# Optimization experiments

Hardware: AMD Instinct MI355X
Metric: run time of the kernel (lower is better)

The kernel has to match this reference:

```python
import jax, jax.numpy as jnp
import numpy as np

N = 12288
IN_DIM = 256
OUT_DIM = 128
NEG_SLOPE = 0.01  # torch nn.LeakyReLU default


def setup_inputs() -> dict:
    key = jax.random.key(0)
    k1, k2, k3, k4, k5 = jax.random.split(key, 5)
    adj_mx = jax.random.randint(k1, (N, N), 0, 2, dtype=jnp.int32)
    input_features = jax.random.normal(k2, (N, IN_DIM), dtype=jnp.float32)
    # Linear(in_dim, out_dim): weight [out, in], bias [out]
    W = jax.random.normal(k3, (OUT_DIM, IN_DIM), dtype=jnp.float32) / np.sqrt(IN_DIM)
    b = jax.random.normal(k4, (OUT_DIM,), dtype=jnp.float32) * 0.01
    phi = jax.random.normal(k5, (2 * OUT_DIM, 1), dtype=jnp.float32)
    return {"adj_mx": adj_mx, "input_features": input_features, "W": W, "b": b, "phi": phi}


def reference(adj_mx, input_features, W, b, phi):
    # projection (dropout is identity in eval): [N, out]
    new_features = input_features @ W.T + b
    # additive attention halves: (N,1) + (1,N) -> [N,N]
    first_half = new_features @ phi[:OUT_DIM]          # [N,1]
    second_half = (new_features @ phi[OUT_DIM:]).T     # [1,N]
    similarity = jax.nn.leaky_relu(first_half + second_half, NEG_SLOPE)
    # adjacency with self-loops; mask non-edges to -1e20
    adj_hat = adj_mx.astype(jnp.float32) + jnp.eye(adj_mx.shape[0], dtype=jnp.float32)
    masked = jnp.where(adj_hat > 0, similarity, jnp.float32(-1e20))
    att = jax.nn.softmax(masked, axis=1)               # row-wise softmax [N,N]
    out = att @ new_features                           # [N, out]
    return jax.nn.leaky_relu(out, NEG_SLOPE)
```

## Files before the change

### kernel.cpp

```cpp
#include <hip/hip_runtime.h>
#include <hip/hip_bf16.h>

#define N_NODES 12288
#define IN_DIM 256
#define OUT_DIM 128
#define NEG 0.01f
#define LOG2E 1.44269504088896340736f
#define NSPLIT 4
#define JSPAN (N_NODES / NSPLIT)
#define ROWS_PER_BLK 64
#define TILE_J 32
#define NTILES (JSPAN / TILE_J)

typedef __attribute__((ext_vector_type(8))) short short8;
typedef __attribute__((ext_vector_type(4))) float f32x4;

__device__ __forceinline__ float fast_exp2(float x) {
#if __has_builtin(__builtin_amdgcn_exp2f)
  return __builtin_amdgcn_exp2f(x);
#else
  return exp2f(x);
#endif
}

__device__ __forceinline__ unsigned short f2bf(float x) {
  unsigned u = __float_as_uint(x);
  unsigned r = (u + 0x7FFFu + ((u >> 16) & 1u)) >> 16;
  return (unsigned short)r;
}

__global__ __launch_bounds__(256) void k1_proj(
    const float* __restrict__ X, const float* __restrict__ W,
    const float* __restrict__ bias, float* __restrict__ nf,
    unsigned short* __restrict__ Vt) {
  __shared__ float Xs[32][40];
  __shared__ float Ws[32][136];
  const int t = threadIdx.x;
  const int i0 = blockIdx.x * 32;
  const int tx = t & 31, ty = t >> 5;
  float acc[4][4] = {};
  for (int k0 = 0; k0 < IN_DIM; k0 += 32) {
    __syncthreads();
    {
      int r = t >> 3, kq = (t & 7) * 4;
      float4 xv = *(const float4*)&X[(size_t)(i0 + r) * IN_DIM + k0 + kq];
      Xs[kq + 0][r] = xv.x; Xs[kq + 1][r] = xv.y;
      Xs[kq + 2][r] = xv.z; Xs[kq + 3][r] = xv.w;
    }
#pragma unroll
    for (int q = 0; q < 4; ++q) {
      int idx = t + q * 256;
      int c = idx >> 3, kq = (idx & 7) * 4;
      float4 wv = *(const float4*)&W[(size_t)c * IN_DIM + k0 + kq];
      Ws[kq + 0][c] = wv.x; Ws[kq + 1][c] = wv.y;
      Ws[kq + 2][c] = wv.z; Ws[kq + 3][c] = wv.w;
    }
    __syncthreads();
#pragma unroll
    for (int kk = 0; kk < 32; ++kk) {
      float4 a = *(const float4*)&Xs[kk][ty * 4];
      float4 bv = *(const float4*)&Ws[kk][tx * 4];
      float av[4] = {a.x, a.y, a.z, a.w};
      float bw[4] = {bv.x, bv.y, bv.z, bv.w};
#pragma unroll
      for (int r = 0; r < 4; ++r)
#pragma unroll
        for (int c = 0; c < 4; ++c) acc[r][c] += av[r] * bw[c];
    }
  }
  float4 bv = *(const float4*)&bias[tx * 4];
  float bb[4] = {bv.x, bv.y, bv.z, bv.w};
#pragma unroll
  for (int r = 0; r < 4; ++r) {
    int i = i0 + ty * 4 + r;
    float o[4];
#pragma unroll
    for (int c = 0; c < 4; ++c) {
      o[c] = acc[r][c] + bb[c];
      Vt[(size_t)(tx * 4 + c) * N_NODES + i] = f2bf(o[c]);
    }
    *(float4*)&nf[(size_t)i * OUT_DIM + tx * 4] = *(float4*)o;
  }
}

__global__ __launch_bounds__(64) void k2_fs(
    const float* __restrict__ nf, const float* __restrict__ phi,
    float* __restrict__ f, float* __restrict__ s, unsigned* __restrict__ smax) {
  const int i = blockIdx.x, l = threadIdx.x;
  float2 v = *(const float2*)&nf[(size_t)i * OUT_DIM + 2 * l];
  float2 p1 = *(const float2*)&phi[2 * l];
  float2 p2 = *(const float2*)&phi[OUT_DIM + 2 * l];
  float fp = v.x * p1.x + v.y * p1.y;
  float sp = v.x * p2.x + v.y * p2.y;
#pragma unroll
  for (int o = 32; o; o >>= 1) {
    fp += __shfl_xor(fp, o);
    sp += __shfl_xor(sp, o);
  }
  if (l == 0) {
    f[i] = fp; s[i] = sp;
    unsigned u = __float_as_uint(sp);
    unsigned key = (u & 0x80000000u) ? ~u : (u | 0x80000000u);
    atomicMax(smax, key);
  }
}

__global__ __launch_bounds__(256) void k3_attn(
    const int* __restrict__ adj, const unsigned short* __restrict__ Vt,
    const float* __restrict__ f, const float* __restrict__ s,
    const unsigned* __restrict__ smaxk,
    float* __restrict__ pacc, float* __restrict__ pden) {
  __shared__ float s_lds[JSPAN];
  __shared__ __align__(16) unsigned short Vt_lds[128 * 40];
  __shared__ __align__(16) unsigned short P_lds[64 * 40];
  __shared__ float den_lds[64][4];
  const int t = threadIdx.x;
  const int sp = blockIdx.x & (NSPLIT - 1);
  const int rb = blockIdx.x >> 2;
  const int j0g = sp * JSPAN;
  const int i_loc = t >> 2, jg = t & 3;
  const int i = rb * ROWS_PER_BLK + i_loc;
#pragma unroll
  for (int q = 0; q < 3; ++q) {
    int idx = (t + q * 256) * 4;
    *(float4*)&s_lds[idx] = *(const float4*)&s[j0g + idx];
  }
  unsigned key = *smaxk;
  unsigned u = (key & 0x80000000u) ? (key ^ 0x80000000u) : ~key;
  const float smaxv = __uint_as_float(u);
  const float fi = f[i];
  const float xm = fi + smaxv;
  const float m = fmaxf(xm, NEG * xm);
  const float em = m * LOG2E;
  const int diag_loc = i - j0g;
  float dsum = 0.f;
  f32x4 acc[4][2] = {};
  const int w = t >> 6, l = t & 63;
  const int slot = 8 * (l >> 4);
  const int sd = t >> 1, sh = (t & 1) * 16;
  const unsigned short* vsrc_base = Vt + (size_t)sd * N_NODES + j0g + sh;
  unsigned short* vdst = &Vt_lds[sd * 40 + sh];
  const int* adj_base = adj + (size_t)i * N_NODES + j0g + jg * 8;
  __syncthreads();
  for (int tile = 0; tile < NTILES; ++tile) {
    const int jl0 = tile * TILE_J;
    int4 v0 = *(const int4*)(vsrc_base + jl0);
    int4 v1 = *(const int4*)(vsrc_base + jl0 + 8);
    *(int4*)vdst = v0;
    *(int4*)(vdst + 8) = v1;
    const int jl = jl0 + jg * 8;
    int4 a0 = *(const int4*)(adj_base + jl0);
    int4 a1 = *(const int4*)(adj_base + jl0 + 4);
    float4 sA = *(const float4*)&s_lds[jl];
    float4 sB = *(const float4*)&s_lds[jl + 4];
    const int adjv[8] = {a0.x, a0.y, a0.z, a0.w, a1.x, a1.y, a1.z, a1.w};
    const float sv[8] = {sA.x, sA.y, sA.z, sA.w, sB.x, sB.y, sB.z, sB.w};
    short8 pv;
#pragma unroll
    for (int q = 0; q < 8; ++q) {
      float x = fi + sv[q];
      float xl = fmaxf(x, NEG * x);
      float e = fast_exp2(__builtin_fmaf(xl, LOG2E, -em));
      bool edge = (adjv[q] > 0) || ((jl + q) == diag_loc);
      float p = edge ? e : 0.f;
      dsum += p;
      pv[q] = (short)f2bf(p);
    }
    *(short8*)&P_lds[i_loc * 40 + 8 * jg] = pv;
    __syncthreads();
    short8 af[4];
#pragma unroll
    for (int mt = 0; mt < 4; ++mt)
      af[mt] = *(const short8*)&P_lds[(16 * mt + (l & 15)) * 40 + slot];
#pragma unroll
    for (int nt = 0; nt < 2; ++nt) {
      short8 bfr = *(const short8*)&Vt_lds[(32 * w + 16 * nt + (l & 15)) * 40 + slot];
#pragma unroll
      for (int mt = 0; mt < 4; ++mt)
        acc[mt][nt] = __builtin_amdgcn_mfma_f32_16x16x32_bf16(af[mt], bfr, acc[mt][nt], 0, 0, 0);
    }
    __syncthreads();
  }
  den_lds[i_loc][jg] = dsum;
  __syncthreads();
  if (t < 64) {
    pden[sp * N_NODES + rb * ROWS_PER_BLK + t] =
        den_lds[t][0] + den_lds[t][1] + den_lds[t][2] + den_lds[t][3];
  }
  float* pa = pacc + (size_t)sp * N_NODES * OUT_DIM;
#pragma unroll
  for (int mt = 0; mt < 4; ++mt)
#pragma unroll
    for (int nt = 0; nt < 2; ++nt)
#pragma unroll
      for (int r = 0; r < 4; ++r) {
        int ii = rb * ROWS_PER_BLK + 16 * mt + (l >> 4) * 4 + r;
        int d = 32 * w + 16 * nt + (l & 15);
        pa[(size_t)ii * OUT_DIM + d] = acc[mt][nt][r];
      }
}

__global__ __launch_bounds__(256) void k4_comb(
    const float* __restrict__ pacc, const float* __restrict__ pden,
    float* __restrict__ out) {
  int idx = blockIdx.x * 256 + threadIdx.x;
  int i = idx >> 7;
  float v = 0.f, den = 0.f;
#pragma unroll
  for (int spp = 0; spp < NSPLIT; ++spp) {
    v += pacc[(size_t)spp * N_NODES * OUT_DIM + idx];
    den += pden[spp * N_NODES + i];
  }
  float o = v / den;
  out[idx] = fmaxf(o, NEG * o);
}

extern "C" void kernel_launch(void* const* d_in, const int* in_sizes, int n_in,
                              void* d_out, int out_size, void* d_ws, size_t ws_size,
                              hipStream_t stream) {
  const int* adj = (const int*)d_in[0];
  const float* X = (const float*)d_in[1];
  const float* W = (const float*)d_in[2];
  const float* b = (const float*)d_in[3];
  const float* phi = (const float*)d_in[4];
  float* out = (float*)d_out;
  char* ws = (char*)d_ws;
  unsigned short* Vt = (unsigned short*)(ws);
  float* nf   = (float*)(ws + 3145728);
  float* fv   = (float*)(ws + 9437184);
  float* sv   = (float*)(ws + 9486336);
  unsigned* smax = (unsigned*)(ws + 9535488);
  float* pden = (float*)(ws + 9535504);
  float* pacc = (float*)(ws + 9732112);

  hipMemsetAsync(smax, 0, 4, stream);
  hipLaunchKernelGGL(k1_proj, dim3(N_NODES / 32), dim3(256), 0, stream, X, W, b, nf, Vt);
  hipLaunchKernelGGL(k2_fs, dim3(N_NODES), dim3(64), 0, stream, nf, phi, fv, sv, smax);
  hipLaunchKernelGGL(k3_attn, dim3((N_NODES / ROWS_PER_BLK) * NSPLIT), dim3(256), 0, stream,
                     adj, Vt, fv, sv, smax, pacc, pden);
  hipLaunchKernelGGL(k4_comb, dim3((N_NODES * OUT_DIM) / 256), dim3(256), 0, stream,
                     pacc, pden, out);
}
```

Baseline: 1.024 ms.

## Fuse attention-score projection into k1 and software-pipeline the attention kernel

Folds the f/s dot products with phi and the smax reduction into the projection kernel, which removes the k2 launch and the fp32 nf round trip through memory. The attention kernel is restructured so each wave computes its own 16 rows' P fragments directly in registers, with no P staging in LDS. It also double-buffers Vt tiles of 64 columns, prefetches adjacency two tiles ahead with a three-set register rotation, and uses one barrier per tile. The cost is higher register pressure (launch bounds 256,3) and unrolled code that is more complex.

```diff
diff --git a/kernel.cpp b/kernel.cpp
--- a/kernel.cpp
+++ b/kernel.cpp
@@ -8,9 +8,9 @@
 #define LOG2E 1.44269504088896340736f
 #define NSPLIT 4
 #define JSPAN (N_NODES / NSPLIT)
-#define ROWS_PER_BLK 64
-#define TILE_J 32
-#define NTILES (JSPAN / TILE_J)
+#define TJ 64
+#define NT (JSPAN / TJ)
+#define VROW 68
 
 typedef __attribute__((ext_vector_type(8))) short short8;
 typedef __attribute__((ext_vector_type(4))) float f32x4;
@@ -31,10 +31,12 @@
 
 __global__ __launch_bounds__(256) void k1_proj(
     const float* __restrict__ X, const float* __restrict__ W,
-    const float* __restrict__ bias, float* __restrict__ nf,
-    unsigned short* __restrict__ Vt) {
+    const float* __restrict__ bias, const float* __restrict__ phi,
+    unsigned short* __restrict__ Vt, float* __restrict__ f,
+    float* __restrict__ s, unsigned* __restrict__ smax) {
   __shared__ float Xs[32][40];
   __shared__ float Ws[32][136];
+  __shared__ unsigned skey[8];
   const int t = threadIdx.x;
   const int i0 = blockIdx.x * 32;
   const int tx = t & 31, ty = t >> 5;
@@ -70,134 +72,173 @@
   }
   float4 bv = *(const float4*)&bias[tx * 4];
   float bb[4] = {bv.x, bv.y, bv.z, bv.w};
+  float4 p1 = *(const float4*)&phi[tx * 4];
+  float4 p2 = *(const float4*)&phi[OUT_DIM + tx * 4];
+  float p1a[4] = {p1.x, p1.y, p1.z, p1.w};
+  float p2a[4] = {p2.x, p2.y, p2.z, p2.w};
+  float fp[4], sp_[4];
 #pragma unroll
   for (int r = 0; r < 4; ++r) {
     int i = i0 + ty * 4 + r;
     float o[4];
+    fp[r] = 0.f; sp_[r] = 0.f;
 #pragma unroll
     for (int c = 0; c < 4; ++c) {
       o[c] = acc[r][c] + bb[c];
       Vt[(size_t)(tx * 4 + c) * N_NODES + i] = f2bf(o[c]);
-    }
-    *(float4*)&nf[(size_t)i * OUT_DIM + tx * 4] = *(float4*)o;
-  }
-}
-
-__global__ __launch_bounds__(64) void k2_fs(
-    const float* __restrict__ nf, const float* __restrict__ phi,
-    float* __restrict__ f, float* __restrict__ s, unsigned* __restrict__ smax) {
-  const int i = blockIdx.x, l = threadIdx.x;
-  float2 v = *(const float2*)&nf[(size_t)i * OUT_DIM + 2 * l];
-  float2 p1 = *(const float2*)&phi[2 * l];
-  float2 p2 = *(const float2*)&phi[OUT_DIM + 2 * l];
-  float fp = v.x * p1.x + v.y * p1.y;
-  float sp = v.x * p2.x + v.y * p2.y;
-#pragma unroll
-  for (int o = 32; o; o >>= 1) {
-    fp += __shfl_xor(fp, o);
-    sp += __shfl_xor(sp, o);
-  }
-  if (l == 0) {
-    f[i] = fp; s[i] = sp;
-    unsigned u = __float_as_uint(sp);
-    unsigned key = (u & 0x80000000u) ? ~u : (u | 0x80000000u);
-    atomicMax(smax, key);
-  }
-}
-
-__global__ __launch_bounds__(256) void k3_attn(
+      fp[r] = __builtin_fmaf(o[c], p1a[c], fp[r]);
+      sp_[r] = __builtin_fmaf(o[c], p2a[c], sp_[r]);
+    }
+  }
+#pragma unroll
+  for (int o = 16; o; o >>= 1) {
+#pragma unroll
+    for (int r = 0; r < 4; ++r) {
+      fp[r] += __shfl_xor(fp[r], o);
+      sp_[r] += __shfl_xor(sp_[r], o);
+    }
+  }
+  if (tx == 0) {
+    unsigned kmax = 0;
+#pragma unroll
+    for (int r = 0; r < 4; ++r) {
+      int i = i0 + ty * 4 + r;
+      f[i] = fp[r]; s[i] = sp_[r];
+      unsigned u = __float_as_uint(sp_[r]);
+      unsigned key = (u & 0x80000000u) ? ~u : (u | 0x80000000u);
+      kmax = max(kmax, key);
+    }
+    skey[ty] = kmax;
+  }
+  __syncthreads();
+  if (t == 0) {
+    unsigned kmax = skey[0];
+#pragma unroll
+    for (int q = 1; q < 8; ++q) kmax = max(kmax, skey[q]);
+    atomicMax(smax, kmax);
+  }
+}
+
+__global__ __launch_bounds__(256, 3) void k3_attn(
     const int* __restrict__ adj, const unsigned short* __restrict__ Vt,
     const float* __restrict__ f, const float* __restrict__ s,
     const unsigned* __restrict__ smaxk,
     float* __restrict__ pacc, float* __restrict__ pden) {
   __shared__ float s_lds[JSPAN];
-  __shared__ __align__(16) unsigned short Vt_lds[128 * 40];
-  __shared__ __align__(16) unsigned short P_lds[64 * 40];
-  __shared__ float den_lds[64][4];
+  __shared__ __align__(16) unsigned short Vt_lds[2][128 * VROW];
   const int t = threadIdx.x;
   const int sp = blockIdx.x & (NSPLIT - 1);
   const int rb = blockIdx.x >> 2;
   const int j0g = sp * JSPAN;
-  const int i_loc = t >> 2, jg = t & 3;
-  const int i = rb * ROWS_PER_BLK + i_loc;
+  const int w = t >> 6, l = t & 63;
+  const int m = l & 15, slot = l >> 4;
+  const int row_g = rb * 64 + w * 16 + m;
 #pragma unroll
   for (int q = 0; q < 3; ++q) {
     int idx = (t + q * 256) * 4;
     *(float4*)&s_lds[idx] = *(const float4*)&s[j0g + idx];
   }
   unsigned key = *smaxk;
-  unsigned u = (key & 0x80000000u) ? (key ^ 0x80000000u) : ~key;
-  const float smaxv = __uint_as_float(u);
-  const float fi = f[i];
+  unsigned ku = (key & 0x80000000u) ? (key ^ 0x80000000u) : ~key;
+  const float smaxv = __uint_as_float(ku);
+  const float fi = f[row_g];
   const float xm = fi + smaxv;
-  const float m = fmaxf(xm, NEG * xm);
-  const float em = m * LOG2E;
-  const int diag_loc = i - j0g;
+  const float mrow = fmaxf(xm, NEG * xm);
+  const float em = mrow * LOG2E;
+  const int diag_g = row_g - j0g;
   float dsum = 0.f;
-  f32x4 acc[4][2] = {};
-  const int w = t >> 6, l = t & 63;
-  const int slot = 8 * (l >> 4);
-  const int sd = t >> 1, sh = (t & 1) * 16;
-  const unsigned short* vsrc_base = Vt + (size_t)sd * N_NODES + j0g + sh;
-  unsigned short* vdst = &Vt_lds[sd * 40 + sh];
-  const int* adj_base = adj + (size_t)i * N_NODES + j0g + jg * 8;
+  f32x4 acc[8] = {};
+  const int* adjp = adj + (size_t)row_g * N_NODES + j0g + 8 * slot;
+  const int sd = t >> 1, sh = (t & 1) * 32;
+  const unsigned short* vsrc = Vt + (size_t)sd * N_NODES + j0g + sh;
+  unsigned short* vd0 = &Vt_lds[0][sd * VROW + sh];
+  unsigned short* vd1 = &Vt_lds[1][sd * VROW + sh];
+  int4 aA[4], aB[4], aC[4], vr[4];
+
+#define ADJ_LOAD(SET, TT) { int _o = (TT) * TJ;                       \
+    SET[0] = *(const int4*)(adjp + _o);                               \
+    SET[1] = *(const int4*)(adjp + _o + 4);                           \
+    SET[2] = *(const int4*)(adjp + _o + 32);                          \
+    SET[3] = *(const int4*)(adjp + _o + 36); }
+#define VT_LOAD(TT) { int _o = (TT) * TJ;                             \
+    vr[0] = *(const int4*)(vsrc + _o);                                \
+    vr[1] = *(const int4*)(vsrc + _o + 8);                            \
+    vr[2] = *(const int4*)(vsrc + _o + 16);                           \
+    vr[3] = *(const int4*)(vsrc + _o + 24); }
+#define VT_WRITE(DST) { *(int4*)(DST) = vr[0]; *(int4*)((DST) + 8) = vr[1]; \
+    *(int4*)((DST) + 16) = vr[2]; *(int4*)((DST) + 24) = vr[3]; }
+
+  VT_LOAD(0);
+  ADJ_LOAD(aA, 0);
+  ADJ_LOAD(aB, 1);
+  VT_WRITE(vd0);
   __syncthreads();
-  for (int tile = 0; tile < NTILES; ++tile) {
-    const int jl0 = tile * TILE_J;
-    int4 v0 = *(const int4*)(vsrc_base + jl0);
-    int4 v1 = *(const int4*)(vsrc_base + jl0 + 8);
-    *(int4*)vdst = v0;
-    *(int4*)(vdst + 8) = v1;
-    const int jl = jl0 + jg * 8;
-    int4 a0 = *(const int4*)(adj_base + jl0);
-    int4 a1 = *(const int4*)(adj_base + jl0 + 4);
-    float4 sA = *(const float4*)&s_lds[jl];
-    float4 sB = *(const float4*)&s_lds[jl + 4];
-    const int adjv[8] = {a0.x, a0.y, a0.z, a0.w, a1.x, a1.y, a1.z, a1.w};
-    const float sv[8] = {sA.x, sA.y, sA.z, sA.w, sB.x, sB.y, sB.z, sB.w};
-    short8 pv;
-#pragma unroll
-    for (int q = 0; q < 8; ++q) {
-      float x = fi + sv[q];
-      float xl = fmaxf(x, NEG * x);
-      float e = fast_exp2(__builtin_fmaf(xl, LOG2E, -em));
-      bool edge = (adjv[q] > 0) || ((jl + q) == diag_loc);
-      float p = edge ? e : 0.f;
-      dsum += p;
-      pv[q] = (short)f2bf(p);
-    }
-    *(short8*)&P_lds[i_loc * 40 + 8 * jg] = pv;
-    __syncthreads();
-    short8 af[4];
-#pragma unroll
-    for (int mt = 0; mt < 4; ++mt)
-      af[mt] = *(const short8*)&P_lds[(16 * mt + (l & 15)) * 40 + slot];
-#pragma unroll
-    for (int nt = 0; nt < 2; ++nt) {
-      short8 bfr = *(const short8*)&Vt_lds[(32 * w + 16 * nt + (l & 15)) * 40 + slot];
-#pragma unroll
-      for (int mt = 0; mt < 4; ++mt)
-        acc[mt][nt] = __builtin_amdgcn_mfma_f32_16x16x32_bf16(af[mt], bfr, acc[mt][nt], 0, 0, 0);
-    }
-    __syncthreads();
-  }
-  den_lds[i_loc][jg] = dsum;
-  __syncthreads();
-  if (t < 64) {
-    pden[sp * N_NODES + rb * ROWS_PER_BLK + t] =
-        den_lds[t][0] + den_lds[t][1] + den_lds[t][2] + den_lds[t][3];
-  }
+  int cur = 0;
+
+#define ITER(TT, CURSET, PFSET) {                                           \
+    int _tn = ((TT) + 1 < NT) ? (TT) + 1 : NT - 1;                          \
+    VT_LOAD(_tn);                            \
+    int _tp = ((TT) + 2 < NT) ? (TT) + 2 : NT - 1;                          \
+    ADJ_LOAD(PFSET, _tp);                  \
+    short8 af0, af1;                                                        \
+    _Pragma("unroll")                                                       \
+    for (int c = 0; c < 2; ++c) {                                           \
+      int jb = (TT) * TJ + 32 * c + 8 * slot;                               \
+      float4 sv0 = *(const float4*)&s_lds[jb];                              \
+      float4 sv1 = *(const float4*)&s_lds[jb + 4];                          \
+      int av[8] = {CURSET[2*c].x, CURSET[2*c].y, CURSET[2*c].z, CURSET[2*c].w, \
+                   CURSET[2*c+1].x, CURSET[2*c+1].y, CURSET[2*c+1].z, CURSET[2*c+1].w}; \
+      float sva[8] = {sv0.x, sv0.y, sv0.z, sv0.w, sv1.x, sv1.y, sv1.z, sv1.w}; \
+      _Pragma("unroll")                                                     \
+      for (int q = 0; q < 8; ++q) {                                         \
+        float x = fi + sva[q];                                              \
+        float xl = fmaxf(x, NEG * x);                                       \
+        float e = fast_exp2(__builtin_fmaf(xl, LOG2E, -em));                \
+        bool edge = (av[q] > 0) || ((jb + q) == diag_g);                    \
+        float p = edge ? e : 0.f;                                           \
+        dsum += p;                                                          \
+        if (c == 0) af0[q] = (short)f2bf(p); else af1[q] = (short)f2bf(p);  \
+      }                                                                     \
+    }                                                                       \
+    const unsigned short* vb = &Vt_lds[cur][0];                             \
+    _Pragma("unroll")                                                       \
+    for (int nt = 0; nt < 8; ++nt) {                                        \
+      short8 b0 = *(const short8*)(vb + (nt * 16 + m) * VROW + 8 * slot);   \
+      acc[nt] = __builtin_amdgcn_mfma_f32_16x16x32_bf16(af0, b0, acc[nt], 0, 0, 0); \
+    }                                                                       \
+    _Pragma("unroll")                                                       \
+    for (int nt = 0; nt < 8; ++nt) {                                        \
+      short8 b1 = *(const short8*)(vb + (nt * 16 + m) * VROW + 32 + 8 * slot); \
+      acc[nt] = __builtin_amdgcn_mfma_f32_16x16x32_bf16(af1, b1, acc[nt], 0, 0, 0); \
+    }                                                                       \
+    unsigned short* vw = (cur ? vd0 : vd1);                                 \
+    VT_WRITE(vw);                          \
+    asm volatile("s_waitcnt lgkmcnt(0)" ::: "memory");                      \
+    __builtin_amdgcn_sched_barrier(0);                                      \
+    __builtin_amdgcn_s_barrier();                                           \
+    cur ^= 1; }
+
+  for (int tb = 0; tb < NT; tb += 3) {
+    ITER(tb + 0, aA, aC);
+    ITER(tb + 1, aB, aA);
+    ITER(tb + 2, aC, aB);
+  }
+#undef ITER
+#undef ADJ_LOAD
+#undef VT_LOAD
+#undef VT_WRITE
+
+  dsum += __shfl_xor(dsum, 16);
+  dsum += __shfl_xor(dsum, 32);
+  if (l < 16) pden[sp * N_NODES + rb * 64 + w * 16 + l] = dsum;
   float* pa = pacc + (size_t)sp * N_NODES * OUT_DIM;
 #pragma unroll
-  for (int mt = 0; mt < 4; ++mt)
-#pragma unroll
-    for (int nt = 0; nt < 2; ++nt)
-#pragma unroll
-      for (int r = 0; r < 4; ++r) {
-        int ii = rb * ROWS_PER_BLK + 16 * mt + (l >> 4) * 4 + r;
-        int d = 32 * w + 16 * nt + (l & 15);
-        pa[(size_t)ii * OUT_DIM + d] = acc[mt][nt][r];
-      }
+  for (int nt = 0; nt < 8; ++nt)
+#pragma unroll
+    for (int r = 0; r < 4; ++r) {
+      int ii = rb * 64 + w * 16 + slot * 4 + r;
+      pa[(size_t)ii * OUT_DIM + nt * 16 + m] = acc[nt][r];
+    }
 }
 
 __global__ __launch_bounds__(256) void k4_comb(
@@ -226,17 +267,16 @@
   float* out = (float*)d_out;
   char* ws = (char*)d_ws;
   unsigned short* Vt = (unsigned short*)(ws);
-  float* nf   = (float*)(ws + 3145728);
-  float* fv   = (float*)(ws + 9437184);
-  float* sv   = (float*)(ws + 9486336);
-  unsigned* smax = (unsigned*)(ws + 9535488);
-  float* pden = (float*)(ws + 9535504);
-  float* pacc = (float*)(ws + 9732112);
+  float* fv   = (float*)(ws + 3145728);
+  float* sv   = (float*)(ws + 3194880);
+  unsigned* smax = (unsigned*)(ws + 3244032);
+  float* pden = (float*)(ws + 3244048);
+  float* pacc = (float*)(ws + 3440656);
 
   hipMemsetAsync(smax, 0, 4, stream);
-  hipLaunchKernelGGL(k1_proj, dim3(N_NODES / 32), dim3(256), 0, stream, X, W, b, nf, Vt);
-  hipLaunchKernelGGL(k2_fs, dim3(N_NODES), dim3(64), 0, stream, nf, phi, fv, sv, smax);
-  hipLaunchKernelGGL(k3_attn, dim3((N_NODES / ROWS_PER_BLK) * NSPLIT), dim3(256), 0, stream,
+  hipLaunchKernelGGL(k1_proj, dim3(N_NODES / 32), dim3(256), 0, stream,
+                     X, W, b, phi, Vt, fv, sv, smax);
+  hipLaunchKernelGGL(k3_attn, dim3((N_NODES / 64) * NSPLIT), dim3(256), 0, stream,
                      adj, Vt, fv, sv, smax, pacc, pden);
   hipLaunchKernelGGL(k4_comb, dim3((N_NODES * OUT_DIM) / 256), dim3(256), 0, stream,
                      pacc, pden, out);
```

New measurement: 990.9 us. -3.3%, faster.
